# Performance work log

Measured on AMD Instinct MI355X. Metric: run time of the kernel, lower is better.

## Reference

```python
import jax, jax.numpy as jnp
import numpy as np

N0, N1, N2 = 120000, 30000, 6000   # node frontier sizes per hop
E0, E1 = 480000, 96000             # sampled edges per layer (~fanout 16)
D = 128                            # in_channels == hidden_size
R = 8                              # num_relations
NB = 4                             # num_bases
ETOT = 3000000                     # global edge count (edge_type_all)


def setup_inputs() -> dict:
    key = jax.random.key(0)
    ks = jax.random.split(key, 24)
    s = 1.0 / np.sqrt(D)
    f32 = jnp.float32
    inp = {
        "x": jax.random.normal(ks[0], (N0, D), dtype=f32),
        "src0": jax.random.randint(ks[1], (E0,), 0, N0),
        "dst0": jax.random.randint(ks[2], (E0,), 0, N1),
        "e_id0": jax.random.randint(ks[3], (E0,), 0, ETOT),
        "src1": jax.random.randint(ks[4], (E1,), 0, N1),
        "dst1": jax.random.randint(ks[5], (E1,), 0, N2),
        "e_id1": jax.random.randint(ks[6], (E1,), 0, ETOT),
        "edge_type_all": jax.random.randint(ks[7], (ETOT,), 0, R),
        # pre_layer: linear + relu
        "pre_W": jax.random.normal(ks[8], (D, D), dtype=f32) * s,
        "pre_b": jnp.zeros((D,), f32),
        # RGCNConv layer 0 (basis decomposition)
        "basis0": jax.random.normal(ks[9], (NB, D, D), dtype=f32) * s,
        "comp0": jax.random.normal(ks[10], (R, NB), dtype=f32) * (1.0 / np.sqrt(NB)),
        "root0": jax.random.normal(ks[11], (D, D), dtype=f32) * s,
        "bias0": jnp.zeros((D,), f32),
        "g0": jnp.ones((D,), f32),
        "be0": jnp.zeros((D,), f32),
        # RGCNConv layer 1
        "basis1": jax.random.normal(ks[12], (NB, D, D), dtype=f32) * s,
        "comp1": jax.random.normal(ks[13], (R, NB), dtype=f32) * (1.0 / np.sqrt(NB)),
        "root1": jax.random.normal(ks[14], (D, D), dtype=f32) * s,
        "bias1": jnp.zeros((D,), f32),
        "g1": jnp.ones((D,), f32),
        "be1": jnp.zeros((D,), f32),
        # post_layer: single linear
        "post_W": jax.random.normal(ks[15], (D, D), dtype=f32) * s,
        "post_b": jnp.zeros((D,), f32),
    }
    return inp


def _layernorm(x, g, b, eps=1e-5):
    mu = jnp.mean(x, axis=-1, keepdims=True)
    var = jnp.mean(jnp.square(x - mu), axis=-1, keepdims=True)
    return (x - mu) * jax.lax.rsqrt(var + eps) * g + b


def _rgcn_conv(x, n_dst, src, dst, etype, basis, comp, root, bias):
    # Bipartite RGCNConv with basis decomposition and mean aggregation.
    # Since messages W[r] @ x[src] are linear, aggregate per relation first
    # (segment_sum of raw features), then apply the relation weight once.
    x_t = x[:n_dst]                                    # [n_dst, D]
    out = x_t @ root + bias                            # root/self transform
    W = jnp.einsum('rb,bio->rio', comp, basis)         # [R, D, D]
    x_j = x[src]                                       # [E, D] gather
    deg = jax.ops.segment_sum(jnp.ones(src.shape[0], x.dtype), dst,
                              num_segments=n_dst)      # mean over all relations
    agg = jnp.zeros((n_dst, W.shape[-1]), x.dtype)
    for r in range(W.shape[0]):                        # R=8 structurally distinct
        m = (etype == r).astype(x.dtype)[:, None]
        s_r = jax.ops.segment_sum(x_j * m, dst, num_segments=n_dst)
        agg = agg + s_r @ W[r]
    return out + agg / jnp.maximum(deg, 1.0)[:, None]


def reference(x, src0, dst0, e_id0, src1, dst1, e_id1, edge_type_all,
              pre_W, pre_b, basis0, comp0, root0, bias0, g0, be0,
              basis1, comp1, root1, bias1, g1, be1, post_W, post_b):
    # pre_layer: linear + relu (GeneralMultiLayer, final_act=True)
    h = jax.nn.relu(x @ pre_W + pre_b)
    # layer 0: edge-type gather -> relational conv -> norm -> act (eval: no dropout)
    h = _rgcn_conv(h, N1, src0, dst0, edge_type_all[e_id0],
                   basis0, comp0, root0, bias0)
    h = jax.nn.relu(_layernorm(h, g0, be0))
    # layer 1
    h = _rgcn_conv(h, N2, src1, dst1, edge_type_all[e_id1],
                   basis1, comp1, root1, bias1)
    h = jax.nn.relu(_layernorm(h, g1, be1))
    # post_layer: single linear MLP
    return h @ post_W + post_b
```

## Files before the change

### kernel.cpp

```cpp
#include <hip/hip_runtime.h>
#include <cstdint>

#define DD 128
#define CAP 64
#define E0C 480000
#define E1C 96000
#define N0C 120000
#define N1C 30000
#define N2C 6000
#define ETOTC 3000000
#define FSLICE 2250

typedef unsigned short u16;
typedef __attribute__((ext_vector_type(8))) short bf16x8;
typedef __attribute__((ext_vector_type(16))) float f32x16;

__device__ __forceinline__ u16 f2b(float f) {
    union { float f; unsigned u; } a; a.f = f;
    unsigned r = (a.u + 0x7fffu + ((a.u >> 16) & 1u)) >> 16;
    return (u16)r;
}
__device__ __forceinline__ float b2f(u16 u) {
    union { unsigned u; float f; } a; a.u = ((unsigned)u) << 16;
    return a.f;
}

struct WtJob { const float* src[12]; };
__global__ __launch_bounds__(256) void prep_kernel(
    WtJob job, u16* __restrict__ dst, int* __restrict__ cnt0, int* __restrict__ cnt1,
    const int* __restrict__ etype, unsigned* __restrict__ r4)
{
    int gtid = blockIdx.x * 256 + threadIdx.x;
    for (int i = gtid; i < N1C + N2C; i += 256 * 256) {
        if (i < N1C) cnt0[i] = 0; else cnt1[i - N1C] = 0;
    }
    for (int i = gtid; i < ETOTC / 8; i += 256 * 256) {
        int4 a = ((const int4*)etype)[i * 2];
        int4 b = ((const int4*)etype)[i * 2 + 1];
        unsigned p = (unsigned)(a.x & 7) | ((unsigned)(a.y & 7) << 4)
                   | ((unsigned)(a.z & 7) << 8) | ((unsigned)(a.w & 7) << 12)
                   | ((unsigned)(b.x & 7) << 16) | ((unsigned)(b.y & 7) << 20)
                   | ((unsigned)(b.z & 7) << 24) | ((unsigned)(b.w & 7) << 28);
        r4[i] = p;
    }
    if (blockIdx.x >= 192) return;
    __shared__ float tile[32][33];
    int m = blockIdx.x >> 4;
    int t4 = blockIdx.x & 15;
    int tr = (t4 >> 2) * 32;
    int tc = (t4 & 3) * 32;
    int lx = threadIdx.x & 31, ly = threadIdx.x >> 5;
    #pragma unroll
    for (int yy = 0; yy < 32; yy += 8)
        tile[ly + yy][lx] = job.src[m][(tr + ly + yy) * DD + tc + lx];
    __syncthreads();
    int tid = threadIdx.x;
    if (tid < 128) {
        int nl = tid >> 2, kch = tid & 3;
        int k = tr + kch * 8, n = tc + nl;
        int kc = k >> 4, half = (k >> 3) & 1;
        int t = n >> 5, l31 = n & 31;
        bf16x8 pk;
        #pragma unroll
        for (int j = 0; j < 8; ++j) pk[j] = (short)f2b(tile[kch * 8 + j][nl]);
        *(bf16x8*)(dst + (size_t)m * 16384 + kc * 2048 + t * 512 + half * 256 + l31 * 8) = pk;
    }
}

__global__ __launch_bounds__(256) void fill_kernel(
    const int* __restrict__ src0, const int* __restrict__ dst0, const int* __restrict__ eid0,
    const int* __restrict__ src1, const int* __restrict__ dst1, const int* __restrict__ eid1,
    const unsigned* __restrict__ r4,
    int* __restrict__ cnt0, int* __restrict__ cnt1,
    int* __restrict__ ep0, int* __restrict__ ep1)
{
    int part  = blockIdx.x & 7;
    int slice = blockIdx.x >> 3;
    int lo0 = part * (N1C / 8), hi0 = lo0 + N1C / 8;
    int lo1 = part * (N2C / 8), hi1 = lo1 + N2C / 8;
    int base = slice * FSLICE;
    for (int t = threadIdx.x; t < FSLICE; t += 256) {
        int idx = base + t;
        bool L0 = idx < E0C;
        int ee = L0 ? idx : idx - E0C;
        int d   = L0 ? dst0[ee] : dst1[ee];
        int s   = L0 ? src0[ee] : src1[ee];
        int eid = L0 ? eid0[ee] : eid1[ee];
        bool mine = L0 ? (d >= lo0 && d < hi0) : (d >= lo1 && d < hi1);
        if (!mine) continue;
        int r = (int)((r4[eid >> 3] >> ((eid & 7) << 2)) & 7u);
        int pos = atomicAdd((L0 ? cnt0 : cnt1) + d, 1);
        if (pos < CAP)
            (L0 ? ep0 : ep1)[(size_t)d * CAP + pos] = s | (r << 28);
    }
}

__global__ __launch_bounds__(256) void pre_gemm_kernel(
    const float* __restrict__ x, const u16* __restrict__ Wr,
    const float* __restrict__ bias, u16* __restrict__ h0)
{
    int wave = threadIdx.x >> 6;
    int lane = threadIdx.x & 63;
    int l31 = lane & 31, half = lane >> 5;
    int m0 = (blockIdx.x * 4 + wave) * 32;
    if (m0 >= N0C) return;
    int arow = m0 + l31;
    bool rv = arow < N0C;

    const float* Aq = x + (size_t)arow * DD;
    float4 st[16];
    if (rv) {
        #pragma unroll
        for (int c = 0; c < 16; ++c)
            st[c] = *(const float4*)(Aq + ((c >> 1) * 16 + half * 8) + (c & 1) * 4);
    } else {
        #pragma unroll
        for (int c = 0; c < 16; ++c) st[c] = make_float4(0.f, 0.f, 0.f, 0.f);
    }
    f32x16 accs[4];
    #pragma unroll
    for (int t = 0; t < 4; ++t)
        #pragma unroll
        for (int i = 0; i < 16; ++i) accs[t][i] = 0.f;
    #pragma unroll
    for (int kc = 0; kc < 8; ++kc) {
        bf16x8 bfr[4];
        #pragma unroll
        for (int t = 0; t < 4; ++t)
            bfr[t] = *(const bf16x8*)(Wr + (size_t)((kc * 4 + t) * 64 + lane) * 8);
        float4 u0 = st[2 * kc], u1 = st[2 * kc + 1];
        bf16x8 af;
        af[0] = (short)f2b(u0.x); af[1] = (short)f2b(u0.y);
        af[2] = (short)f2b(u0.z); af[3] = (short)f2b(u0.w);
        af[4] = (short)f2b(u1.x); af[5] = (short)f2b(u1.y);
        af[6] = (short)f2b(u1.z); af[7] = (short)f2b(u1.w);
        #pragma unroll
        for (int t = 0; t < 4; ++t)
            accs[t] = __builtin_amdgcn_mfma_f32_32x32x16_bf16(af, bfr[t], accs[t], 0, 0, 0);
    }
    float bb[4];
    #pragma unroll
    for (int t = 0; t < 4; ++t) bb[t] = bias[t * 32 + l31];
    #pragma unroll
    for (int reg = 0; reg < 16; ++reg) {
        int rl = (reg & 3) + 8 * (reg >> 2) + 4 * half;
        int row = m0 + rl;
        if (row < N0C) {
            #pragma unroll
            for (int t = 0; t < 4; ++t)
                h0[(size_t)row * DD + t * 32 + l31] =
                    f2b(fmaxf(accs[t][reg] + bb[t], 0.f));
        }
    }
}

__global__ __launch_bounds__(256) void agg_kernel(
    const u16* __restrict__ h, const int* __restrict__ cnt,
    const int* __restrict__ ep, const float* __restrict__ comp,
    u16* __restrict__ T, int ndst)
{
    __shared__ float4 cmp4[8];
    if (threadIdx.x < 8) cmp4[threadIdx.x] = ((const float4*)comp)[threadIdx.x];
    __syncthreads();
    int row = blockIdx.x * 4 + (threadIdx.x >> 6);
    if (row >= ndst) return;
    int lane = threadIdx.x & 63;
    int n = cnt[row];
    int end = n < CAP ? n : CAP;
    const int* erow = ep + (size_t)row * CAP;
    float a0[4] = {0.f, 0.f, 0.f, 0.f};
    float a1[4] = {0.f, 0.f, 0.f, 0.f};
    int j = 0;
    for (; j + 16 <= end; j += 16) {
        int vv[16]; unsigned gg[16];
        #pragma unroll
        for (int u = 0; u < 16; ++u) vv[u] = erow[j + u];
        #pragma unroll
        for (int u = 0; u < 16; ++u)
            gg[u] = *(const unsigned*)(h + (size_t)(vv[u] & 0x0FFFFFFF) * DD + 2 * lane);
        #pragma unroll
        for (int u = 0; u < 16; ++u) {
            float4 c = cmp4[vv[u] >> 28];
            float x0 = b2f((u16)(gg[u] & 0xffffu));
            float x1 = b2f((u16)(gg[u] >> 16));
            a0[0] = fmaf(c.x, x0, a0[0]); a1[0] = fmaf(c.x, x1, a1[0]);
            a0[1] = fmaf(c.y, x0, a0[1]); a1[1] = fmaf(c.y, x1, a1[1]);
            a0[2] = fmaf(c.z, x0, a0[2]); a1[2] = fmaf(c.z, x1, a1[2]);
            a0[3] = fmaf(c.w, x0, a0[3]); a1[3] = fmaf(c.w, x1, a1[3]);
        }
    }
    for (; j + 4 <= end; j += 4) {
        int vv[4]; unsigned gg[4];
        #pragma unroll
        for (int u = 0; u < 4; ++u) vv[u] = erow[j + u];
        #pragma unroll
        for (int u = 0; u < 4; ++u)
            gg[u] = *(const unsigned*)(h + (size_t)(vv[u] & 0x0FFFFFFF) * DD + 2 * lane);
        #pragma unroll
        for (int u = 0; u < 4; ++u) {
            float4 c = cmp4[vv[u] >> 28];
            float x0 = b2f((u16)(gg[u] & 0xffffu));
            float x1 = b2f((u16)(gg[u] >> 16));
            a0[0] = fmaf(c.x, x0, a0[0]); a1[0] = fmaf(c.x, x1, a1[0]);
            a0[1] = fmaf(c.y, x0, a0[1]); a1[1] = fmaf(c.y, x1, a1[1]);
            a0[2] = fmaf(c.z, x0, a0[2]); a1[2] = fmaf(c.z, x1, a1[2]);
            a0[3] = fmaf(c.w, x0, a0[3]); a1[3] = fmaf(c.w, x1, a1[3]);
        }
    }
    for (; j < end; ++j) {
        int v = erow[j];
        unsigned g = *(const unsigned*)(h + (size_t)(v & 0x0FFFFFFF) * DD + 2 * lane);
        float4 c = cmp4[v >> 28];
        float x0 = b2f((u16)(g & 0xffffu));
        float x1 = b2f((u16)(g >> 16));
        a0[0] = fmaf(c.x, x0, a0[0]); a1[0] = fmaf(c.x, x1, a1[0]);
        a0[1] = fmaf(c.y, x0, a0[1]); a1[1] = fmaf(c.y, x1, a1[1]);
        a0[2] = fmaf(c.z, x0, a0[2]); a1[2] = fmaf(c.z, x1, a1[2]);
        a0[3] = fmaf(c.w, x0, a0[3]); a1[3] = fmaf(c.w, x1, a1[3]);
    }
    float inv = 1.f / fmaxf((float)n, 1.f);
    #pragma unroll
    for (int b = 0; b < 4; ++b) {
        unsigned pk = (unsigned)f2b(a0[b] * inv) | ((unsigned)f2b(a1[b] * inv) << 16);
        *(unsigned*)(T + ((size_t)b * ndst + row) * DD + 2 * lane) = pk;
    }
}

template<bool OBF16, bool LN>
__global__ __launch_bounds__(64) void mfma_gemm(
    const u16* __restrict__ Ap, int nplanes, const u16* __restrict__ Ar,
    const u16* __restrict__ Wp, const u16* __restrict__ Wr,
    const float* __restrict__ bias, const float* __restrict__ gw,
    const float* __restrict__ bw, void* __restrict__ Cv, int nrows)
{
    int lane = threadIdx.x & 63;
    int l31 = lane & 31, half = lane >> 5;
    int m0 = blockIdx.x * 32;
    int arow = m0 + l31;
    bool rv = arow < nrows;
    f32x16 acc[4];
    #pragma unroll
    for (int t = 0; t < 4; ++t)
        #pragma unroll
        for (int i = 0; i < 16; ++i) acc[t][i] = 0.f;

    bf16x8 A0[8], A1[8];
    {
        const u16* Ainit = (nplanes == 0) ? Ar : Ap;
        if (rv) {
            #pragma unroll
            for (int c = 0; c < 8; ++c)
                A0[c] = *(const bf16x8*)(Ainit + (size_t)arow * DD + c * 16 + half * 8);
        } else {
            #pragma unroll
            for (int c = 0; c < 8; ++c) A0[c] = (bf16x8){0,0,0,0,0,0,0,0};
        }
    }
    for (int p = 0; p <= nplanes; ++p) {
        const u16* Wsel = (p == nplanes) ? Wr : Wp + p * 16384;
        if (p < nplanes) {
            const u16* An = (p + 1 == nplanes) ? Ar : Ap + (size_t)(p + 1) * nrows * DD;
            if (rv) {
                #pragma unroll
                for (int c = 0; c < 8; ++c)
                    A1[c] = *(const bf16x8*)(An + (size_t)arow * DD + c * 16 + half * 8);
            } else {
                #pragma unroll
                for (int c = 0; c < 8; ++c) A1[c] = (bf16x8){0,0,0,0,0,0,0,0};
            }
        }
        #pragma unroll
        for (int kc = 0; kc < 8; ++kc) {
            bf16x8 bfr[4];
            #pragma unroll
            for (int t = 0; t < 4; ++t)
                bfr[t] = *(const bf16x8*)(Wsel + (size_t)((kc * 4 + t) * 64 + lane) * 8);
            #pragma unroll
            for (int t = 0; t < 4; ++t)
                acc[t] = __builtin_amdgcn_mfma_f32_32x32x16_bf16(A0[kc], bfr[t], acc[t], 0, 0, 0);
        }
        if (p < nplanes) {
            #pragma unroll
            for (int c = 0; c < 8; ++c) A0[c] = A1[c];
        }
    }

    float bb[4];
    #pragma unroll
    for (int t = 0; t < 4; ++t) bb[t] = bias[t * 32 + l31];
    float gg[4], ww[4];
    if (LN) {
        #pragma unroll
        for (int t = 0; t < 4; ++t) { gg[t] = gw[t * 32 + l31]; ww[t] = bw[t * 32 + l31]; }
    }

    #pragma unroll
    for (int reg = 0; reg < 16; ++reg) {
        int rl = (reg & 3) + 8 * (reg >> 2) + 4 * half;
        int row = m0 + rl;
        float v[4];
        #pragma unroll
        for (int t = 0; t < 4; ++t) v[t] = acc[t][reg] + bb[t];
        if (LN) {
            float s1 = 0.f, s2 = 0.f;
            #pragma unroll
            for (int t = 0; t < 4; ++t) { s1 += v[t]; s2 += v[t] * v[t]; }
            #pragma unroll
            for (int o = 1; o < 32; o <<= 1) {
                s1 += __shfl_xor(s1, o);
                s2 += __shfl_xor(s2, o);
            }
            float mu = s1 * (1.f / 128.f);
            float var = s2 * (1.f / 128.f) - mu * mu;
            float rstd = rsqrtf(fmaxf(var, 0.f) + 1e-5f);
            #pragma unroll
            for (int t = 0; t < 4; ++t)
                v[t] = fmaxf((v[t] - mu) * rstd * gg[t] + ww[t], 0.f);
        }
        if (row < nrows) {
            #pragma unroll
            for (int t = 0; t < 4; ++t) {
                if (OBF16) ((u16*)Cv)[(size_t)row * DD + t * 32 + l31] = f2b(v[t]);
                else       ((float*)Cv)[(size_t)row * DD + t * 32 + l31] = v[t];
            }
        }
    }
}

extern "C" void kernel_launch(void* const* d_in, const int* in_sizes, int n_in,
                              void* d_out, int out_size, void* d_ws, size_t ws_size,
                              hipStream_t stream)
{
    const float* x     = (const float*)d_in[0];
    const int* src0    = (const int*)d_in[1];
    const int* dst0    = (const int*)d_in[2];
    const int* eid0    = (const int*)d_in[3];
    const int* src1    = (const int*)d_in[4];
    const int* dst1    = (const int*)d_in[5];
    const int* eid1    = (const int*)d_in[6];
    const int* etype   = (const int*)d_in[7];
    const float* preW  = (const float*)d_in[8];
    const float* preb  = (const float*)d_in[9];
    const float* basis0 = (const float*)d_in[10];
    const float* comp0  = (const float*)d_in[11];
    const float* root0  = (const float*)d_in[12];
    const float* bias0  = (const float*)d_in[13];
    const float* g0    = (const float*)d_in[14];
    const float* be0   = (const float*)d_in[15];
    const float* basis1 = (const float*)d_in[16];
    const float* comp1  = (const float*)d_in[17];
    const float* root1  = (const float*)d_in[18];
    const float* bias1  = (const float*)d_in[19];
    const float* g1    = (const float*)d_in[20];
    const float* be1   = (const float*)d_in[21];
    const float* postW = (const float*)d_in[22];
    const float* postb = (const float*)d_in[23];
    float* out = (float*)d_out;

    char* ws = (char*)d_ws;
    size_t o = 0;
    auto alloc = [&](size_t bytes) { char* p = ws + o; o += (bytes + 255) & ~(size_t)255; return p; };
    u16* h0   = (u16*)alloc((size_t)N0C * DD * 2);
    u16* T0   = (u16*)alloc((size_t)4 * N1C * DD * 2);
    u16* h1   = (u16*)alloc((size_t)N1C * DD * 2);
    u16* T1   = (u16*)alloc((size_t)4 * N2C * DD * 2);
    u16* h2   = (u16*)alloc((size_t)N2C * DD * 2);
    u16* wt   = (u16*)alloc((size_t)12 * 16384 * 2);
    int* cnt0 = (int*)alloc((size_t)N1C * 4);
    int* cnt1 = (int*)alloc((size_t)N2C * 4);
    int* ep0  = (int*)alloc((size_t)N1C * CAP * 4);
    int* ep1  = (int*)alloc((size_t)N2C * CAP * 4);
    unsigned* r4 = (unsigned*)alloc((size_t)(ETOTC / 8) * 4);

    WtJob job;
    job.src[0] = preW;
    for (int b = 0; b < 4; ++b) job.src[1 + b] = basis0 + (size_t)b * 16384;
    job.src[5] = root0;
    for (int b = 0; b < 4; ++b) job.src[6 + b] = basis1 + (size_t)b * 16384;
    job.src[10] = root1;
    job.src[11] = postW;

    prep_kernel<<<256, 256, 0, stream>>>(job, wt, cnt0, cnt1, etype, r4);
    fill_kernel<<<2048, 256, 0, stream>>>(
        src0, dst0, eid0, src1, dst1, eid1, r4, cnt0, cnt1, ep0, ep1);
    pre_gemm_kernel<<<(N0C + 127) / 128, 256, 0, stream>>>(
        x, wt + 0 * 16384, preb, h0);
    agg_kernel<<<(N1C + 3) / 4, 256, 0, stream>>>(h0, cnt0, ep0, comp0, T0, N1C);
    mfma_gemm<true, true><<<(N1C + 31) / 32, 64, 0, stream>>>(
        T0, 4, h0, wt + 1 * 16384, wt + 5 * 16384, bias0, g0, be0, h1, N1C);
    agg_kernel<<<(N2C + 3) / 4, 256, 0, stream>>>(h1, cnt1, ep1, comp1, T1, N2C);
    mfma_gemm<true, true><<<(N2C + 31) / 32, 64, 0, stream>>>(
        T1, 4, h1, wt + 6 * 16384, wt + 10 * 16384, bias1, g1, be1, h2, N2C);
    mfma_gemm<false, false><<<(N2C + 31) / 32, 64, 0, stream>>>(
        nullptr, 0, h2, nullptr, wt + 11 * 16384, postb, nullptr, nullptr, out, N2C);
}
```

Baseline: 299.4 us.

## Merge fill with pre-GEMM launch and fuse post linear into layer-1 GEMM

The edge-fill kernel and the pre-layer GEMM now share one launch, with the block index choosing which role a block runs, so the two independent jobs can overlap on the device. The layer-1 RGCN GEMM with LayerNorm now stages its bf16 output tile in shared memory and applies the post linear in the same kernel, which removes the h2 round trip and one launch. The LN GEMM is also specialised to four basis planes, with the template flags removed. The cost is a larger combined kernel with mixed block roles, and the fused kernel needs extra registers and LDS.

New measurement: 283.7 us. 5.2% less time.

```diff
diff --git a/kernel.cpp b/kernel.cpp
--- a/kernel.cpp
+++ b/kernel.cpp
@@ -10,6 +10,7 @@
 #define N2C 6000
 #define ETOTC 3000000
 #define FSLICE 2250
+#define FILLB 2048
 
 typedef unsigned short u16;
 typedef __attribute__((ext_vector_type(8))) short bf16x8;
@@ -67,42 +68,44 @@
     }
 }
 
-__global__ __launch_bounds__(256) void fill_kernel(
+__global__ __launch_bounds__(256) void fillpre_kernel(
+    const float* __restrict__ x,
     const int* __restrict__ src0, const int* __restrict__ dst0, const int* __restrict__ eid0,
     const int* __restrict__ src1, const int* __restrict__ dst1, const int* __restrict__ eid1,
     const unsigned* __restrict__ r4,
     int* __restrict__ cnt0, int* __restrict__ cnt1,
-    int* __restrict__ ep0, int* __restrict__ ep1)
+    int* __restrict__ ep0, int* __restrict__ ep1,
+    const u16* __restrict__ Wr, const float* __restrict__ bias,
+    u16* __restrict__ h0)
 {
-    int part  = blockIdx.x & 7;
-    int slice = blockIdx.x >> 3;
-    int lo0 = part * (N1C / 8), hi0 = lo0 + N1C / 8;
-    int lo1 = part * (N2C / 8), hi1 = lo1 + N2C / 8;
-    int base = slice * FSLICE;
-    for (int t = threadIdx.x; t < FSLICE; t += 256) {
-        int idx = base + t;
-        bool L0 = idx < E0C;
-        int ee = L0 ? idx : idx - E0C;
-        int d   = L0 ? dst0[ee] : dst1[ee];
-        int s   = L0 ? src0[ee] : src1[ee];
-        int eid = L0 ? eid0[ee] : eid1[ee];
-        bool mine = L0 ? (d >= lo0 && d < hi0) : (d >= lo1 && d < hi1);
-        if (!mine) continue;
-        int r = (int)((r4[eid >> 3] >> ((eid & 7) << 2)) & 7u);
-        int pos = atomicAdd((L0 ? cnt0 : cnt1) + d, 1);
-        if (pos < CAP)
-            (L0 ? ep0 : ep1)[(size_t)d * CAP + pos] = s | (r << 28);
-    }
-}
-
-__global__ __launch_bounds__(256) void pre_gemm_kernel(
-    const float* __restrict__ x, const u16* __restrict__ Wr,
-    const float* __restrict__ bias, u16* __restrict__ h0)
-{
+    if (blockIdx.x < FILLB) {
+        int part  = blockIdx.x & 7;
+        int slice = blockIdx.x >> 3;
+        int lo0 = part * (N1C / 8), hi0 = lo0 + N1C / 8;
+        int lo1 = part * (N2C / 8), hi1 = lo1 + N2C / 8;
+        int base = slice * FSLICE;
+        for (int t = threadIdx.x; t < FSLICE; t += 256) {
+            int idx = base + t;
+            bool L0 = idx < E0C;
+            int ee = L0 ? idx : idx - E0C;
+            int d   = L0 ? dst0[ee] : dst1[ee];
+            int s   = L0 ? src0[ee] : src1[ee];
+            int eid = L0 ? eid0[ee] : eid1[ee];
+            bool mine = L0 ? (d >= lo0 && d < hi0) : (d >= lo1 && d < hi1);
+            if (!mine) continue;
+            int r = (int)((r4[eid >> 3] >> ((eid & 7) << 2)) & 7u);
+            int pos = atomicAdd((L0 ? cnt0 : cnt1) + d, 1);
+            if (pos < CAP)
+                (L0 ? ep0 : ep1)[(size_t)d * CAP + pos] = s | (r << 28);
+        }
+        return;
+    }
+
+    int bid = blockIdx.x - FILLB;
     int wave = threadIdx.x >> 6;
     int lane = threadIdx.x & 63;
     int l31 = lane & 31, half = lane >> 5;
-    int m0 = (blockIdx.x * 4 + wave) * 32;
+    int m0 = (bid * 4 + wave) * 32;
     if (m0 >= N0C) return;
     int arow = m0 + l31;
     bool rv = arow < N0C;
@@ -226,12 +229,11 @@
     }
 }
 
-template<bool OBF16, bool LN>
-__global__ __launch_bounds__(64) void mfma_gemm(
-    const u16* __restrict__ Ap, int nplanes, const u16* __restrict__ Ar,
+__global__ __launch_bounds__(64) void mfma_gemm_ln(
+    const u16* __restrict__ Ap, const u16* __restrict__ Ar,
     const u16* __restrict__ Wp, const u16* __restrict__ Wr,
     const float* __restrict__ bias, const float* __restrict__ gw,
-    const float* __restrict__ bw, void* __restrict__ Cv, int nrows)
+    const float* __restrict__ bw, u16* __restrict__ Cv, int nrows)
 {
     int lane = threadIdx.x & 63;
     int l31 = lane & 31, half = lane >> 5;
@@ -245,21 +247,18 @@
         for (int i = 0; i < 16; ++i) acc[t][i] = 0.f;
 
     bf16x8 A0[8], A1[8];
-    {
-        const u16* Ainit = (nplanes == 0) ? Ar : Ap;
-        if (rv) {
-            #pragma unroll
-            for (int c = 0; c < 8; ++c)
-                A0[c] = *(const bf16x8*)(Ainit + (size_t)arow * DD + c * 16 + half * 8);
-        } else {
-            #pragma unroll
-            for (int c = 0; c < 8; ++c) A0[c] = (bf16x8){0,0,0,0,0,0,0,0};
-        }
-    }
-    for (int p = 0; p <= nplanes; ++p) {
-        const u16* Wsel = (p == nplanes) ? Wr : Wp + p * 16384;
-        if (p < nplanes) {
-            const u16* An = (p + 1 == nplanes) ? Ar : Ap + (size_t)(p + 1) * nrows * DD;
+    if (rv) {
+        #pragma unroll
+        for (int c = 0; c < 8; ++c)
+            A0[c] = *(const bf16x8*)(Ap + (size_t)arow * DD + c * 16 + half * 8);
+    } else {
+        #pragma unroll
+        for (int c = 0; c < 8; ++c) A0[c] = (bf16x8){0,0,0,0,0,0,0,0};
+    }
+    for (int p = 0; p <= 4; ++p) {
+        const u16* Wsel = (p == 4) ? Wr : Wp + (size_t)p * 16384;
+        if (p < 4) {
+            const u16* An = (p + 1 == 4) ? Ar : Ap + (size_t)(p + 1) * nrows * DD;
             if (rv) {
                 #pragma unroll
                 for (int c = 0; c < 8; ++c)
@@ -279,21 +278,19 @@
             for (int t = 0; t < 4; ++t)
                 acc[t] = __builtin_amdgcn_mfma_f32_32x32x16_bf16(A0[kc], bfr[t], acc[t], 0, 0, 0);
         }
-        if (p < nplanes) {
+        if (p < 4) {
             #pragma unroll
             for (int c = 0; c < 8; ++c) A0[c] = A1[c];
         }
     }
 
-    float bb[4];
-    #pragma unroll
-    for (int t = 0; t < 4; ++t) bb[t] = bias[t * 32 + l31];
-    float gg[4], ww[4];
-    if (LN) {
-        #pragma unroll
-        for (int t = 0; t < 4; ++t) { gg[t] = gw[t * 32 + l31]; ww[t] = bw[t * 32 + l31]; }
-    }
-
+    float bb[4], gg[4], ww[4];
+    #pragma unroll
+    for (int t = 0; t < 4; ++t) {
+        bb[t] = bias[t * 32 + l31];
+        gg[t] = gw[t * 32 + l31];
+        ww[t] = bw[t * 32 + l31];
+    }
     #pragma unroll
     for (int reg = 0; reg < 16; ++reg) {
         int rl = (reg & 3) + 8 * (reg >> 2) + 4 * half;
@@ -301,28 +298,144 @@
         float v[4];
         #pragma unroll
         for (int t = 0; t < 4; ++t) v[t] = acc[t][reg] + bb[t];
-        if (LN) {
-            float s1 = 0.f, s2 = 0.f;
-            #pragma unroll
-            for (int t = 0; t < 4; ++t) { s1 += v[t]; s2 += v[t] * v[t]; }
-            #pragma unroll
-            for (int o = 1; o < 32; o <<= 1) {
-                s1 += __shfl_xor(s1, o);
-                s2 += __shfl_xor(s2, o);
+        float s1 = 0.f, s2 = 0.f;
+        #pragma unroll
+        for (int t = 0; t < 4; ++t) { s1 += v[t]; s2 += v[t] * v[t]; }
+        #pragma unroll
+        for (int o = 1; o < 32; o <<= 1) {
+            s1 += __shfl_xor(s1, o);
+            s2 += __shfl_xor(s2, o);
+        }
+        float mu = s1 * (1.f / 128.f);
+        float var = s2 * (1.f / 128.f) - mu * mu;
+        float rstd = rsqrtf(fmaxf(var, 0.f) + 1e-5f);
+        if (row < nrows) {
+            #pragma unroll
+            for (int t = 0; t < 4; ++t)
+                Cv[(size_t)row * DD + t * 32 + l31] =
+                    f2b(fmaxf((v[t] - mu) * rstd * gg[t] + ww[t], 0.f));
+        }
+    }
+}
+
+__global__ __launch_bounds__(64) void gemm_post_kernel(
+    const u16* __restrict__ Ap, const u16* __restrict__ Ar,
+    const u16* __restrict__ Wp, const u16* __restrict__ Wr,
+    const float* __restrict__ bias, const float* __restrict__ gw,
+    const float* __restrict__ bw,
+    const u16* __restrict__ Wpost, const float* __restrict__ postb,
+    float* __restrict__ outp, int nrows)
+{
+    __shared__ u16 lt[32][136];
+    int lane = threadIdx.x & 63;
+    int l31 = lane & 31, half = lane >> 5;
+    int m0 = blockIdx.x * 32;
+    int arow = m0 + l31;
+    bool rv = arow < nrows;
+    f32x16 acc[4];
+    #pragma unroll
+    for (int t = 0; t < 4; ++t)
+        #pragma unroll
+        for (int i = 0; i < 16; ++i) acc[t][i] = 0.f;
+
+    bf16x8 A0[8], A1[8];
+    if (rv) {
+        #pragma unroll
+        for (int c = 0; c < 8; ++c)
+            A0[c] = *(const bf16x8*)(Ap + (size_t)arow * DD + c * 16 + half * 8);
+    } else {
+        #pragma unroll
+        for (int c = 0; c < 8; ++c) A0[c] = (bf16x8){0,0,0,0,0,0,0,0};
+    }
+    for (int p = 0; p <= 4; ++p) {
+        const u16* Wsel = (p == 4) ? Wr : Wp + (size_t)p * 16384;
+        if (p < 4) {
+            const u16* An = (p + 1 == 4) ? Ar : Ap + (size_t)(p + 1) * nrows * DD;
+            if (rv) {
+                #pragma unroll
+                for (int c = 0; c < 8; ++c)
+                    A1[c] = *(const bf16x8*)(An + (size_t)arow * DD + c * 16 + half * 8);
+            } else {
+                #pragma unroll
+                for (int c = 0; c < 8; ++c) A1[c] = (bf16x8){0,0,0,0,0,0,0,0};
             }
-            float mu = s1 * (1.f / 128.f);
-            float var = s2 * (1.f / 128.f) - mu * mu;
-            float rstd = rsqrtf(fmaxf(var, 0.f) + 1e-5f);
-            #pragma unroll
-            for (int t = 0; t < 4; ++t)
-                v[t] = fmaxf((v[t] - mu) * rstd * gg[t] + ww[t], 0.f);
-        }
+        }
+        #pragma unroll
+        for (int kc = 0; kc < 8; ++kc) {
+            bf16x8 bfr[4];
+            #pragma unroll
+            for (int t = 0; t < 4; ++t)
+                bfr[t] = *(const bf16x8*)(Wsel + (size_t)((kc * 4 + t) * 64 + lane) * 8);
+            #pragma unroll
+            for (int t = 0; t < 4; ++t)
+                acc[t] = __builtin_amdgcn_mfma_f32_32x32x16_bf16(A0[kc], bfr[t], acc[t], 0, 0, 0);
+        }
+        if (p < 4) {
+            #pragma unroll
+            for (int c = 0; c < 8; ++c) A0[c] = A1[c];
+        }
+    }
+
+    float bb[4], gg[4], ww[4];
+    #pragma unroll
+    for (int t = 0; t < 4; ++t) {
+        bb[t] = bias[t * 32 + l31];
+        gg[t] = gw[t * 32 + l31];
+        ww[t] = bw[t * 32 + l31];
+    }
+    #pragma unroll
+    for (int reg = 0; reg < 16; ++reg) {
+        int rl = (reg & 3) + 8 * (reg >> 2) + 4 * half;
+        float v[4];
+        #pragma unroll
+        for (int t = 0; t < 4; ++t) v[t] = acc[t][reg] + bb[t];
+        float s1 = 0.f, s2 = 0.f;
+        #pragma unroll
+        for (int t = 0; t < 4; ++t) { s1 += v[t]; s2 += v[t] * v[t]; }
+        #pragma unroll
+        for (int o = 1; o < 32; o <<= 1) {
+            s1 += __shfl_xor(s1, o);
+            s2 += __shfl_xor(s2, o);
+        }
+        float mu = s1 * (1.f / 128.f);
+        float var = s2 * (1.f / 128.f) - mu * mu;
+        float rstd = rsqrtf(fmaxf(var, 0.f) + 1e-5f);
+        #pragma unroll
+        for (int t = 0; t < 4; ++t)
+            lt[rl][t * 32 + l31] = f2b(fmaxf((v[t] - mu) * rstd * gg[t] + ww[t], 0.f));
+    }
+    __syncthreads();
+
+    f32x16 acc2[4];
+    #pragma unroll
+    for (int t = 0; t < 4; ++t)
+        #pragma unroll
+        for (int i = 0; i < 16; ++i) acc2[t][i] = 0.f;
+    bf16x8 A[8];
+    #pragma unroll
+    for (int c = 0; c < 8; ++c)
+        A[c] = *(const bf16x8*)&lt[l31][c * 16 + half * 8];
+    #pragma unroll
+    for (int kc = 0; kc < 8; ++kc) {
+        bf16x8 bfr[4];
+        #pragma unroll
+        for (int t = 0; t < 4; ++t)
+            bfr[t] = *(const bf16x8*)(Wpost + (size_t)((kc * 4 + t) * 64 + lane) * 8);
+        #pragma unroll
+        for (int t = 0; t < 4; ++t)
+            acc2[t] = __builtin_amdgcn_mfma_f32_32x32x16_bf16(A[kc], bfr[t], acc2[t], 0, 0, 0);
+    }
+    float pb[4];
+    #pragma unroll
+    for (int t = 0; t < 4; ++t) pb[t] = postb[t * 32 + l31];
+    #pragma unroll
+    for (int reg = 0; reg < 16; ++reg) {
+        int rl = (reg & 3) + 8 * (reg >> 2) + 4 * half;
+        int row = m0 + rl;
         if (row < nrows) {
             #pragma unroll
-            for (int t = 0; t < 4; ++t) {
-                if (OBF16) ((u16*)Cv)[(size_t)row * DD + t * 32 + l31] = f2b(v[t]);
-                else       ((float*)Cv)[(size_t)row * DD + t * 32 + l31] = v[t];
-            }
+            for (int t = 0; t < 4; ++t)
+                outp[(size_t)row * DD + t * 32 + l31] = acc2[t][reg] + pb[t];
         }
     }
 }
@@ -364,7 +477,6 @@
     u16* T0   = (u16*)alloc((size_t)4 * N1C * DD * 2);
     u16* h1   = (u16*)alloc((size_t)N1C * DD * 2);
     u16* T1   = (u16*)alloc((size_t)4 * N2C * DD * 2);
-    u16* h2   = (u16*)alloc((size_t)N2C * DD * 2);
     u16* wt   = (u16*)alloc((size_t)12 * 16384 * 2);
     int* cnt0 = (int*)alloc((size_t)N1C * 4);
     int* cnt1 = (int*)alloc((size_t)N2C * 4);
@@ -381,16 +493,14 @@
     job.src[11] = postW;
 
     prep_kernel<<<256, 256, 0, stream>>>(job, wt, cnt0, cnt1, etype, r4);
-    fill_kernel<<<2048, 256, 0, stream>>>(
-        src0, dst0, eid0, src1, dst1, eid1, r4, cnt0, cnt1, ep0, ep1);
-    pre_gemm_kernel<<<(N0C + 127) / 128, 256, 0, stream>>>(
-        x, wt + 0 * 16384, preb, h0);
+    fillpre_kernel<<<FILLB + (N0C + 127) / 128, 256, 0, stream>>>(
+        x, src0, dst0, eid0, src1, dst1, eid1, r4,
+        cnt0, cnt1, ep0, ep1, wt + 0 * 16384, preb, h0);
     agg_kernel<<<(N1C + 3) / 4, 256, 0, stream>>>(h0, cnt0, ep0, comp0, T0, N1C);
-    mfma_gemm<true, true><<<(N1C + 31) / 32, 64, 0, stream>>>(
-        T0, 4, h0, wt + 1 * 16384, wt + 5 * 16384, bias0, g0, be0, h1, N1C);
+    mfma_gemm_ln<<<(N1C + 31) / 32, 64, 0, stream>>>(
+        T0, h0, wt + 1 * 16384, wt + 5 * 16384, bias0, g0, be0, h1, N1C);
     agg_kernel<<<(N2C + 3) / 4, 256, 0, stream>>>(h1, cnt1, ep1, comp1, T1, N2C);
-    mfma_gemm<true, true><<<(N2C + 31) / 32, 64, 0, stream>>>(
-        T1, 4, h1, wt + 6 * 16384, wt + 10 * 16384, bias1, g1, be1, h2, N2C);
-    mfma_gemm<false, false><<<(N2C + 31) / 32, 64, 0, stream>>>(
-        nullptr, 0, h2, nullptr, wt + 11 * 16384, postb, nullptr, nullptr, out, N2C);
-}
+    gemm_post_kernel<<<(N2C + 31) / 32, 64, 0, stream>>>(
+        T1, h1, wt + 6 * 16384, wt + 10 * 16384, bias1, g1, be1,
+        wt + 11 * 16384, postb, out, N2C);
+}
```
